# Optimization experiments

Measured on AMD Instinct MI355X. Metric: run time of the kernel, lower is better.

The kernel has to match this reference:

```python
import jax, jax.numpy as jnp
import numpy as np

B, A, T, D = 4, 64, 128, 512
H = 8
DH = D // H
DFF = 4 * D

def layer_norm(x, g, b, eps=1e-5):
    mu = jnp.mean(x, axis=-1, keepdims=True)
    var = jnp.var(x, axis=-1, keepdims=True)
    return (x - mu) * jax.lax.rsqrt(var + eps) * g + b

def setup_inputs() -> dict:
    key = jax.random.key(0)
    ks = jax.random.split(key, 8)
    s = 0.02
    return {
        "x": jax.random.normal(ks[0], (B, A, T, D), dtype=jnp.float32),
        "ln1_g": jnp.ones((D,), jnp.float32),
        "ln1_b": jnp.zeros((D,), jnp.float32),
        "W_qkv": jax.random.normal(ks[1], (D, 3 * D), jnp.float32) * s,
        "b_qkv": jnp.zeros((3 * D,), jnp.float32),
        "W_proj": jax.random.normal(ks[2], (D, D), jnp.float32) * s,
        "b_proj": jnp.zeros((D,), jnp.float32),
        "ln2_g": jnp.ones((D,), jnp.float32),
        "ln2_b": jnp.zeros((D,), jnp.float32),
        "W_fc": jax.random.normal(ks[3], (D, DFF), jnp.float32) * s,
        "b_fc": jnp.zeros((DFF,), jnp.float32),
        "W_out": jax.random.normal(ks[4], (DFF, D), jnp.float32) * s,
        "b_out": jnp.zeros((D,), jnp.float32),
    }

def reference(x, ln1_g, ln1_b, W_qkv, b_qkv, W_proj, b_proj,
              ln2_g, ln2_b, W_fc, b_fc, W_out, b_out):
    # pre-norm (note: original adds residual from the NORMED x)
    xn = layer_norm(x, ln1_g, ln1_b)
    # qkv projection: [B,A,T,3D]
    qkv = xn @ W_qkv + b_qkv
    q, k, v = jnp.split(qkv, 3, axis=-1)
    # [B,A,T,H,DH]
    q = q.reshape(B, A, T, H, DH)
    k = k.reshape(B, A, T, H, DH)
    v = v.reshape(B, A, T, H, DH)
    # attention across time, per (batch, agent, head): scores [B,A,H,T,T]
    att = jnp.einsum('bathd,bashd->bahts', q, k) * (1.0 / np.sqrt(DH))
    causal = jnp.tril(jnp.ones((T, T), dtype=bool))
    att = jnp.where(causal, att, -jnp.inf)
    att = jax.nn.softmax(att, axis=-1)
    y = jnp.einsum('bahts,bashd->bathd', att, v).reshape(B, A, T, D)
    y = y @ W_proj + b_proj
    x = xn + y
    # MLP block
    xn2 = layer_norm(x, ln2_g, ln2_b)
    h = jax.nn.gelu(xn2 @ W_fc + b_fc, approximate=False)
    m = h @ W_out + b_out
    return xn2 + m
```

## Files before the change

kernel.cpp:

```cpp
#include <hip/hip_runtime.h>
#include <math.h>

#define DEV static __device__ __forceinline__

typedef unsigned short u16;
typedef __attribute__((ext_vector_type(8))) short short8;
typedef __attribute__((ext_vector_type(4))) float floatx4;

DEV u16 f2bf(float f) {
  unsigned u = __float_as_uint(f);
  unsigned r = u + 0x7FFFu + ((u >> 16) & 1u);
  return (u16)(r >> 16);
}
DEV float bf2f(u16 v) { return __uint_as_float(((unsigned)v) << 16); }

typedef __attribute__((address_space(1))) void gvoid;
typedef __attribute__((address_space(3))) void lvoid;

DEV void gload16(const u16* g, u16* l) {
  __builtin_amdgcn_global_load_lds((gvoid*)g, (lvoid*)l, 16, 0, 0);
}

__global__ __launch_bounds__(256) void tcast_k(const float* __restrict__ in,
                                               u16* __restrict__ out, int K, int N) {
  __shared__ float t[32][33];
  int nb = blockIdx.x * 32, kb = blockIdx.y * 32;
  int tx = threadIdx.x, ty = threadIdx.y;
#pragma unroll
  for (int r = 0; r < 32; r += 8)
    t[r + ty][tx] = in[(long)(kb + r + ty) * N + nb + tx];
  __syncthreads();
#pragma unroll
  for (int r = 0; r < 32; r += 8)
    out[(long)(nb + r + ty) * K + kb + tx] = f2bf(t[tx][r + ty]);
}

template <typename TI>
__global__ __launch_bounds__(256) void ln_k(const TI* __restrict__ x,
                                            const float* __restrict__ g,
                                            const float* __restrict__ b,
                                            u16* __restrict__ xb) {
  const int lane = threadIdx.x & 63, wid = threadIdx.x >> 6;
  const long row = (long)blockIdx.x * 4 + wid;
  float vv[8];
  if constexpr (sizeof(TI) == 4) {
    const float4* xr = (const float4*)((const float*)x + row * 512);
    float4 v0 = xr[lane * 2], v1 = xr[lane * 2 + 1];
    vv[0] = v0.x; vv[1] = v0.y; vv[2] = v0.z; vv[3] = v0.w;
    vv[4] = v1.x; vv[5] = v1.y; vv[6] = v1.z; vv[7] = v1.w;
  } else {
    short8 v = *(const short8*)((const u16*)x + row * 512 + lane * 8);
#pragma unroll
    for (int i = 0; i < 8; ++i) vv[i] = bf2f((u16)v[i]);
  }
  float s = 0.f, q = 0.f;
#pragma unroll
  for (int i = 0; i < 8; ++i) { s += vv[i]; q += vv[i] * vv[i]; }
#pragma unroll
  for (int off = 1; off < 64; off <<= 1) {
    s += __shfl_xor(s, off, 64);
    q += __shfl_xor(q, off, 64);
  }
  float mean = s * (1.f / 512.f);
  float var = q * (1.f / 512.f) - mean * mean;
  float rs = rsqrtf(var + 1e-5f);
  const float4* gp = (const float4*)g;
  const float4* bp = (const float4*)b;
  float4 g0 = gp[lane * 2], g1 = gp[lane * 2 + 1];
  float4 b0 = bp[lane * 2], b1 = bp[lane * 2 + 1];
  float gg[8] = {g0.x, g0.y, g0.z, g0.w, g1.x, g1.y, g1.z, g1.w};
  float bb[8] = {b0.x, b0.y, b0.z, b0.w, b1.x, b1.y, b1.z, b1.w};
  short8 ov;
#pragma unroll
  for (int i = 0; i < 8; ++i)
    ov[i] = (short)f2bf((vv[i] - mean) * rs * gg[i] + bb[i]);
  *(short8*)&xb[row * 512 + lane * 8] = ov;
}

template <int EPI>
__global__ __launch_bounds__(256) void gemm_k(const u16* __restrict__ A,
                                              const u16* __restrict__ Bt,
                                              const float* __restrict__ bias,
                                              const u16* __restrict__ res,
                                              void* __restrict__ out,
                                              int M, int N, int K) {
  __shared__ __align__(16) u16 lA[128 * 32];
  __shared__ __align__(16) u16 lB[128 * 32];
  const int tid = threadIdx.x;
  const int lane = tid & 63, wid = tid >> 6;
  const int lane15 = lane & 15, khi = lane >> 4;
  const int wr = wid >> 1, wc = wid & 1;
  const long rowB = (long)blockIdx.y * 128;
  const long colB = (long)blockIdx.x * 128;

  floatx4 acc[4][4];
#pragma unroll
  for (int m = 0; m < 4; ++m)
#pragma unroll
    for (int n = 0; n < 4; ++n) acc[m][n] = floatx4{0.f, 0.f, 0.f, 0.f};

  for (int kt = 0; kt < K; kt += 32) {
    __syncthreads();
#pragma unroll
    for (int j = 0; j < 2; ++j) {
      int c = j * 256 + tid;
      int r = c >> 2, cq = c & 3;
      gload16(A + (rowB + r) * K + kt + cq * 8, &lA[(j * 256 + wid * 64) * 8]);
    }
#pragma unroll
    for (int j = 0; j < 2; ++j) {
      int c = j * 256 + tid;
      int r = c >> 2, cq = c & 3;
      gload16(Bt + (colB + r) * K + kt + cq * 8, &lB[(j * 256 + wid * 64) * 8]);
    }
    asm volatile("s_waitcnt vmcnt(0)" ::: "memory");
    __syncthreads();

    short8 af[4];
#pragma unroll
    for (int m = 0; m < 4; ++m)
      af[m] = *(const short8*)&lA[(wr * 64 + m * 16 + lane15) * 32 + khi * 8];
#pragma unroll
    for (int n = 0; n < 4; ++n) {
      short8 bfg = *(const short8*)&lB[(wc * 64 + n * 16 + lane15) * 32 + khi * 8];
#pragma unroll
      for (int m = 0; m < 4; ++m)
        acc[m][n] = __builtin_amdgcn_mfma_f32_16x16x32_bf16(af[m], bfg, acc[m][n], 0, 0, 0);
    }
  }

  const long r0 = rowB + wr * 64;
  const long c0 = colB + wc * 64;
#pragma unroll
  for (int m = 0; m < 4; ++m) {
#pragma unroll
    for (int n = 0; n < 4; ++n) {
      long col = c0 + n * 16 + lane15;
      float bv = bias[col];
#pragma unroll
      for (int jj = 0; jj < 4; ++jj) {
        long row = r0 + m * 16 + khi * 4 + jj;
        float v = acc[m][n][jj] + bv;
        if (EPI == 1) v = 0.5f * v * (1.f + erff(v * 0.70710678118f));
        if (EPI == 2 || EPI == 3) v += bf2f(res[row * N + col]);
        if (EPI == 3) {
          ((float*)out)[row * N + col] = v;
        } else {
          ((u16*)out)[row * N + col] = f2bf(v);
        }
      }
    }
  }
}

__global__ __launch_bounds__(256) void attn_k(const u16* __restrict__ qkv,
                                              u16* __restrict__ y) {
  union U {
    struct { u16 q[128 * 64]; u16 k[128 * 64]; } qk;
    u16 p[128 * 128];
  };
  __shared__ __align__(16) U u;
  __shared__ __align__(16) u16 vt[64 * 128];

  const int tid = threadIdx.x;
  const int lane = tid & 63, wid = tid >> 6;
  const int lane15 = lane & 15, khi = lane >> 4;
  const int h = blockIdx.x & 7;
  const long R0 = (long)(blockIdx.x >> 3) * 128;
  const u16* base = qkv + R0 * 1536 + h * 64;

#pragma unroll
  for (int it = 0; it < 4; ++it) {
    int c = it * 256 + tid;
    int r = c >> 3, ch = c & 7;
    const u16* gq = base + (long)r * 1536 + ch * 8;
    uint4 dq = *(const uint4*)gq;
    uint4 dk = *(const uint4*)(gq + 512);
    uint4 dv = *(const uint4*)(gq + 1024);
    int qi = (r * 64 + ch * 8) ^ ((r & 7) << 3);
    *(uint4*)&u.qk.q[qi] = dq;
    *(uint4*)&u.qk.k[qi] = dk;
    u16 tmp[8];
    *(uint4*)tmp = dv;
#pragma unroll
    for (int i = 0; i < 8; ++i) {
      int d = ch * 8 + i;
      vt[(d * 128 + r) ^ ((d & 7) << 3)] = tmp[i];
    }
  }
  __syncthreads();

  const int r0 = wid * 32;
  floatx4 sc[2][8];
#pragma unroll
  for (int mt = 0; mt < 2; ++mt)
#pragma unroll
    for (int c = 0; c < 8; ++c) sc[mt][c] = floatx4{0.f, 0.f, 0.f, 0.f};

#pragma unroll
  for (int kk = 0; kk < 2; ++kk) {
    short8 aq[2];
#pragma unroll
    for (int mt = 0; mt < 2; ++mt) {
      int rr = r0 + mt * 16 + lane15;
      aq[mt] = *(const short8*)&u.qk.q[(rr * 64 + kk * 32 + khi * 8) ^ ((rr & 7) << 3)];
    }
#pragma unroll
    for (int c = 0; c < 8; ++c) {
      int rk = c * 16 + lane15;
      short8 bk = *(const short8*)&u.qk.k[(rk * 64 + kk * 32 + khi * 8) ^ ((rk & 7) << 3)];
#pragma unroll
      for (int mt = 0; mt < 2; ++mt)
        sc[mt][c] = __builtin_amdgcn_mfma_f32_16x16x32_bf16(aq[mt], bk, sc[mt][c], 0, 0, 0);
    }
  }
  __syncthreads();

#pragma unroll
  for (int mt = 0; mt < 2; ++mt) {
#pragma unroll
    for (int jj = 0; jj < 4; ++jj) {
      int t = r0 + mt * 16 + khi * 4 + jj;
      float vals[8];
      float mx = -1e30f;
#pragma unroll
      for (int c = 0; c < 8; ++c) {
        int s = c * 16 + lane15;
        float v = sc[mt][c][jj] * 0.125f;
        vals[c] = (s <= t) ? v : -1e30f;
        mx = fmaxf(mx, vals[c]);
      }
#pragma unroll
      for (int off = 1; off < 16; off <<= 1) mx = fmaxf(mx, __shfl_xor(mx, off, 64));
      float sum = 0.f;
#pragma unroll
      for (int c = 0; c < 8; ++c) {
        float p = __expf(vals[c] - mx);
        vals[c] = p;
        sum += p;
      }
#pragma unroll
      for (int off = 1; off < 16; off <<= 1) sum += __shfl_xor(sum, off, 64);
      float inv = 1.f / sum;
#pragma unroll
      for (int c = 0; c < 8; ++c) {
        int s = c * 16 + lane15;
        u.p[(t * 128 + s) ^ ((t & 7) << 3)] = f2bf(vals[c] * inv);
      }
    }
  }
  __syncthreads();

  floatx4 ya[2][4];
#pragma unroll
  for (int mt = 0; mt < 2; ++mt)
#pragma unroll
    for (int n = 0; n < 4; ++n) ya[mt][n] = floatx4{0.f, 0.f, 0.f, 0.f};

#pragma unroll
  for (int kk = 0; kk < 4; ++kk) {
    short8 ap[2];
#pragma unroll
    for (int mt = 0; mt < 2; ++mt) {
      int rr = r0 + mt * 16 + lane15;
      ap[mt] = *(const short8*)&u.p[(rr * 128 + kk * 32 + khi * 8) ^ ((rr & 7) << 3)];
    }
#pragma unroll
    for (int n = 0; n < 4; ++n) {
      int d = n * 16 + lane15;
      short8 bv = *(const short8*)&vt[(d * 128 + kk * 32 + khi * 8) ^ ((d & 7) << 3)];
#pragma unroll
      for (int mt = 0; mt < 2; ++mt)
        ya[mt][n] = __builtin_amdgcn_mfma_f32_16x16x32_bf16(ap[mt], bv, ya[mt][n], 0, 0, 0);
    }
  }

  u16* yb = y + R0 * 512 + h * 64;
#pragma unroll
  for (int mt = 0; mt < 2; ++mt)
#pragma unroll
    for (int n = 0; n < 4; ++n)
#pragma unroll
      for (int jj = 0; jj < 4; ++jj) {
        int t = r0 + mt * 16 + khi * 4 + jj;
        int d = n * 16 + lane15;
        yb[(long)t * 512 + d] = f2bf(ya[mt][n][jj]);
      }
}

extern "C" void kernel_launch(void* const* d_in, const int* in_sizes, int n_in,
                              void* d_out, int out_size, void* d_ws, size_t ws_size,
                              hipStream_t stream) {
  const float* x      = (const float*)d_in[0];
  const float* ln1_g  = (const float*)d_in[1];
  const float* ln1_b  = (const float*)d_in[2];
  const float* W_qkv  = (const float*)d_in[3];
  const float* b_qkv  = (const float*)d_in[4];
  const float* W_proj = (const float*)d_in[5];
  const float* b_proj = (const float*)d_in[6];
  const float* ln2_g  = (const float*)d_in[7];
  const float* ln2_b  = (const float*)d_in[8];
  const float* W_fc   = (const float*)d_in[9];
  const float* b_fc   = (const float*)d_in[10];
  const float* W_out  = (const float*)d_in[11];
  const float* b_out  = (const float*)d_in[12];

  const size_t MiB = 1024 * 1024;
  char* ws = (char*)d_ws;
  u16* wq   = (u16*)(ws + 0);
  u16* wp   = (u16*)(ws + 1536 * 512 * 2);
  u16* wf   = (u16*)(ws + 2 * MiB);
  u16* wo   = (u16*)(ws + 4 * MiB);
  u16* xnB  = (u16*)(ws + 8 * MiB);
  u16* qkvB = (u16*)(ws + 40 * MiB);
  u16* yB   = (u16*)(ws + 136 * MiB);
  u16* x2B  = (u16*)(ws + 40 * MiB);
  u16* xn2B = (u16*)(ws + 8 * MiB);
  u16* hB   = (u16*)(ws + 40 * MiB);

  const int M = 32768;

  tcast_k<<<dim3(1536 / 32, 512 / 32), dim3(32, 8), 0, stream>>>(W_qkv, wq, 512, 1536);
  tcast_k<<<dim3(512 / 32, 512 / 32), dim3(32, 8), 0, stream>>>(W_proj, wp, 512, 512);
  tcast_k<<<dim3(2048 / 32, 512 / 32), dim3(32, 8), 0, stream>>>(W_fc, wf, 512, 2048);
  tcast_k<<<dim3(512 / 32, 2048 / 32), dim3(32, 8), 0, stream>>>(W_out, wo, 2048, 512);

  ln_k<float><<<M / 4, 256, 0, stream>>>(x, ln1_g, ln1_b, xnB);
  gemm_k<0><<<dim3(1536 / 128, M / 128), 256, 0, stream>>>(xnB, wq, b_qkv, nullptr,
                                                           qkvB, M, 1536, 512);
  attn_k<<<2048, 256, 0, stream>>>(qkvB, yB);
  gemm_k<2><<<dim3(512 / 128, M / 128), 256, 0, stream>>>(yB, wp, b_proj, xnB,
                                                          x2B, M, 512, 512);
  ln_k<u16><<<M / 4, 256, 0, stream>>>(x2B, ln2_g, ln2_b, xn2B);
  gemm_k<1><<<dim3(2048 / 128, M / 128), 256, 0, stream>>>(xn2B, wf, b_fc, nullptr,
                                                           hB, M, 2048, 512);
  gemm_k<3><<<dim3(512 / 128, M / 128), 256, 0, stream>>>(hB, wo, b_out, xn2B,
                                                          (float*)d_out, M, 512, 2048);
}
```

Baseline: 532.5 us.

## Double-buffer GEMM LDS tiles and remap workgroups for XCD locality

Measured after the change: 507.7 us. -4.7%, faster.

```diff
diff --git a/kernel.cpp b/kernel.cpp
--- a/kernel.cpp
+++ b/kernel.cpp
@@ -84,14 +84,27 @@
                                               const u16* __restrict__ res,
                                               void* __restrict__ out,
                                               int M, int N, int K) {
-  __shared__ __align__(16) u16 lA[128 * 32];
-  __shared__ __align__(16) u16 lB[128 * 32];
+  __shared__ __align__(16) u16 lA[2][128 * 32];
+  __shared__ __align__(16) u16 lB[2][128 * 32];
   const int tid = threadIdx.x;
   const int lane = tid & 63, wid = tid >> 6;
   const int lane15 = lane & 15, khi = lane >> 4;
   const int wr = wid >> 1, wc = wid & 1;
-  const long rowB = (long)blockIdx.y * 128;
-  const long colB = (long)blockIdx.x * 128;
+
+  const int gx = gridDim.x;
+  const int nwg = gx * gridDim.y;
+  const int orig = blockIdx.y * gx + blockIdx.x;
+  const int wgid = (orig & 7) * (nwg >> 3) + (orig >> 3);
+  const int bx = wgid % gx;
+  const int by = wgid / gx;
+
+  const long rowB = (long)by * 128;
+  const long colB = (long)bx * 128;
+
+  const int rr = tid >> 2, cq = tid & 3;
+  const u16* gA0 = A + (rowB + rr) * (long)K + cq * 8;
+  const u16* gB0 = Bt + (colB + rr) * (long)K + cq * 8;
+  const long skip = 64 * (long)K;
 
   floatx4 acc[4][4];
 #pragma unroll
@@ -99,34 +112,35 @@
 #pragma unroll
     for (int n = 0; n < 4; ++n) acc[m][n] = floatx4{0.f, 0.f, 0.f, 0.f};
 
-  for (int kt = 0; kt < K; kt += 32) {
-    __syncthreads();
-#pragma unroll
-    for (int j = 0; j < 2; ++j) {
-      int c = j * 256 + tid;
-      int r = c >> 2, cq = c & 3;
-      gload16(A + (rowB + r) * K + kt + cq * 8, &lA[(j * 256 + wid * 64) * 8]);
-    }
-#pragma unroll
-    for (int j = 0; j < 2; ++j) {
-      int c = j * 256 + tid;
-      int r = c >> 2, cq = c & 3;
-      gload16(Bt + (colB + r) * K + kt + cq * 8, &lB[(j * 256 + wid * 64) * 8]);
+  auto stage = [&](int buf, int kt) {
+    gload16(gA0 + kt, &lA[buf][(wid * 64) * 8]);
+    gload16(gA0 + skip + kt, &lA[buf][(256 + wid * 64) * 8]);
+    gload16(gB0 + kt, &lB[buf][(wid * 64) * 8]);
+    gload16(gB0 + skip + kt, &lB[buf][(256 + wid * 64) * 8]);
+  };
+
+  stage(0, 0);
+  asm volatile("s_waitcnt vmcnt(0)" ::: "memory");
+  __syncthreads();
+
+  const int nt = K >> 5;
+  for (int t = 0; t < nt; ++t) {
+    const int cur = t & 1;
+    if (t + 1 < nt) stage(cur ^ 1, (t + 1) << 5);
+    __builtin_amdgcn_sched_barrier(0);
+    short8 af[4];
+#pragma unroll
+    for (int m = 0; m < 4; ++m)
+      af[m] = *(const short8*)&lA[cur][(wr * 64 + m * 16 + lane15) * 32 + khi * 8];
+#pragma unroll
+    for (int n = 0; n < 4; ++n) {
+      short8 bfg = *(const short8*)&lB[cur][(wc * 64 + n * 16 + lane15) * 32 + khi * 8];
+#pragma unroll
+      for (int m = 0; m < 4; ++m)
+        acc[m][n] = __builtin_amdgcn_mfma_f32_16x16x32_bf16(af[m], bfg, acc[m][n], 0, 0, 0);
     }
     asm volatile("s_waitcnt vmcnt(0)" ::: "memory");
     __syncthreads();
-
-    short8 af[4];
-#pragma unroll
-    for (int m = 0; m < 4; ++m)
-      af[m] = *(const short8*)&lA[(wr * 64 + m * 16 + lane15) * 32 + khi * 8];
-#pragma unroll
-    for (int n = 0; n < 4; ++n) {
-      short8 bfg = *(const short8*)&lB[(wc * 64 + n * 16 + lane15) * 32 + khi * 8];
-#pragma unroll
-      for (int m = 0; m < 4; ++m)
-        acc[m][n] = __builtin_amdgcn_mfma_f32_16x16x32_bf16(af[m], bfg, acc[m][n], 0, 0, 0);
-    }
   }
 
   const long r0 = rowB + wr * 64;
```

## Rewrite GEMM as 256x256 tile with 4-stage LDS pipeline and swizzle

Applied to the files above, without the earlier changes.

Measured after the change: 475.7 us. 1.12x faster.

```diff
diff --git a/kernel.cpp b/kernel.cpp
--- a/kernel.cpp
+++ b/kernel.cpp
@@ -78,61 +78,111 @@
 }
 
 template <int EPI>
-__global__ __launch_bounds__(256) void gemm_k(const u16* __restrict__ A,
+__global__ __launch_bounds__(512) void gemm_k(const u16* __restrict__ A,
                                               const u16* __restrict__ Bt,
                                               const float* __restrict__ bias,
                                               const u16* __restrict__ res,
                                               void* __restrict__ out,
                                               int M, int N, int K) {
-  __shared__ __align__(16) u16 lA[128 * 32];
-  __shared__ __align__(16) u16 lB[128 * 32];
+  __shared__ __align__(16) u16 ls[4][2][256 * 32];
   const int tid = threadIdx.x;
-  const int lane = tid & 63, wid = tid >> 6;
+  const int lane = tid & 63, w = tid >> 6;
   const int lane15 = lane & 15, khi = lane >> 4;
-  const int wr = wid >> 1, wc = wid & 1;
-  const long rowB = (long)blockIdx.y * 128;
-  const long colB = (long)blockIdx.x * 128;
-
-  floatx4 acc[4][4];
-#pragma unroll
-  for (int m = 0; m < 4; ++m)
+  const int wr = w >> 2, wcn = w & 3;
+
+  const int gx = gridDim.x;
+  const int nwg = gx * gridDim.y;
+  const int orig = blockIdx.y * gx + blockIdx.x;
+  const int wgid = (orig & 7) * (nwg >> 3) + (orig >> 3);
+  const int bx = wgid % gx, by = wgid / gx;
+  const long rowB = (long)by * 256, colB = (long)bx * 256;
+
+  const int sr = w * 16 + (lane >> 2);
+  const int scb = (lane & 3) * 16;
+
+  auto stageA = [&](int b, int kt) {
+#pragma unroll
+    for (int j = 0; j < 2; ++j) {
+      int r = j * 128 + sr;
+      int sw = ((r >> 1) & 3) << 4;
+      gload16(A + (rowB + r) * (long)K + kt * 32 + ((scb ^ sw) >> 1),
+              &ls[b][0][j * 4096 + w * 512]);
+    }
+  };
+  auto stageB = [&](int b, int kt) {
+#pragma unroll
+    for (int j = 0; j < 2; ++j) {
+      int r = j * 128 + sr;
+      int sw = ((r >> 1) & 3) << 4;
+      gload16(Bt + (colB + r) * (long)K + kt * 32 + ((scb ^ sw) >> 1),
+              &ls[b][1][j * 4096 + w * 512]);
+    }
+  };
+  auto rdA = [&](int b, int m) -> short8 {
+    int r = wr * 128 + m * 16 + lane15;
+    int c8 = (khi ^ ((r >> 1) & 3)) * 8;
+    return *(const short8*)&ls[b][0][r * 32 + c8];
+  };
+  auto rdB = [&](int b, int n) -> short8 {
+    int r = wcn * 64 + n * 16 + lane15;
+    int c8 = (khi ^ ((r >> 1) & 3)) * 8;
+    return *(const short8*)&ls[b][1][r * 32 + c8];
+  };
+
+  floatx4 acc[8][4];
+#pragma unroll
+  for (int m = 0; m < 8; ++m)
 #pragma unroll
     for (int n = 0; n < 4; ++n) acc[m][n] = floatx4{0.f, 0.f, 0.f, 0.f};
 
-  for (int kt = 0; kt < K; kt += 32) {
-    __syncthreads();
-#pragma unroll
-    for (int j = 0; j < 2; ++j) {
-      int c = j * 256 + tid;
-      int r = c >> 2, cq = c & 3;
-      gload16(A + (rowB + r) * K + kt + cq * 8, &lA[(j * 256 + wid * 64) * 8]);
-    }
-#pragma unroll
-    for (int j = 0; j < 2; ++j) {
-      int c = j * 256 + tid;
-      int r = c >> 2, cq = c & 3;
-      gload16(Bt + (colB + r) * K + kt + cq * 8, &lB[(j * 256 + wid * 64) * 8]);
-    }
-    asm volatile("s_waitcnt vmcnt(0)" ::: "memory");
-    __syncthreads();
-
-    short8 af[4];
-#pragma unroll
-    for (int m = 0; m < 4; ++m)
-      af[m] = *(const short8*)&lA[(wr * 64 + m * 16 + lane15) * 32 + khi * 8];
-#pragma unroll
-    for (int n = 0; n < 4; ++n) {
-      short8 bfg = *(const short8*)&lB[(wc * 64 + n * 16 + lane15) * 32 + khi * 8];
+  stageA(0, 0); stageB(0, 0);
+  stageA(1, 1); stageB(1, 1);
+  asm volatile("s_waitcnt vmcnt(4)" ::: "memory");
+  __builtin_amdgcn_s_barrier();
+
+  const int NT = K >> 5;
+  for (int t = 0; t < NT; ++t) {
+    const int b = t & 3;
+    short8 bfr[4], afr[4];
+#pragma unroll
+    for (int n = 0; n < 4; ++n) bfr[n] = rdB(b, n);
+#pragma unroll
+    for (int m = 0; m < 4; ++m) afr[m] = rdA(b, m);
+    if (t + 2 < NT) stageA((t + 2) & 3, t + 2);
+    __builtin_amdgcn_sched_barrier(0);
+    __builtin_amdgcn_s_barrier();
+    __builtin_amdgcn_s_setprio(1);
+#pragma unroll
+    for (int n = 0; n < 4; ++n)
 #pragma unroll
       for (int m = 0; m < 4; ++m)
-        acc[m][n] = __builtin_amdgcn_mfma_f32_16x16x32_bf16(af[m], bfg, acc[m][n], 0, 0, 0);
-    }
-  }
-
-  const long r0 = rowB + wr * 64;
-  const long c0 = colB + wc * 64;
-#pragma unroll
-  for (int m = 0; m < 4; ++m) {
+        acc[m][n] = __builtin_amdgcn_mfma_f32_16x16x32_bf16(afr[m], bfr[n], acc[m][n], 0, 0, 0);
+    __builtin_amdgcn_s_setprio(0);
+    __builtin_amdgcn_s_barrier();
+#pragma unroll
+    for (int m = 0; m < 4; ++m) afr[m] = rdA(b, m + 4);
+    if (t + 2 < NT) stageB((t + 2) & 3, t + 2);
+    __builtin_amdgcn_sched_barrier(0);
+    __builtin_amdgcn_s_barrier();
+    __builtin_amdgcn_s_setprio(1);
+#pragma unroll
+    for (int n = 0; n < 4; ++n)
+#pragma unroll
+      for (int m = 0; m < 4; ++m)
+        acc[m + 4][n] = __builtin_amdgcn_mfma_f32_16x16x32_bf16(afr[m], bfr[n], acc[m + 4][n], 0, 0, 0);
+    __builtin_amdgcn_s_setprio(0);
+    if (t + 2 < NT) {
+      asm volatile("s_waitcnt vmcnt(4)" ::: "memory");
+    } else if (t + 1 < NT) {
+      asm volatile("s_waitcnt vmcnt(0)" ::: "memory");
+    }
+    __builtin_amdgcn_s_barrier();
+  }
+
+  const long r0 = rowB + wr * 128;
+  const long c0 = colB + wcn * 64;
+#pragma unroll
+  for (int m = 0; m < 8; ++m) {
 #pragma unroll
     for (int n = 0; n < 4; ++n) {
       long col = c0 + n * 16 + lane15;
@@ -326,14 +376,14 @@
   tcast_k<<<dim3(512 / 32, 2048 / 32), dim3(32, 8), 0, stream>>>(W_out, wo, 2048, 512);
 
   ln_k<float><<<M / 4, 256, 0, stream>>>(x, ln1_g, ln1_b, xnB);
-  gemm_k<0><<<dim3(1536 / 128, M / 128), 256, 0, stream>>>(xnB, wq, b_qkv, nullptr,
+  gemm_k<0><<<dim3(1536 / 256, M / 256), 512, 0, stream>>>(xnB, wq, b_qkv, nullptr,
                                                            qkvB, M, 1536, 512);
   attn_k<<<2048, 256, 0, stream>>>(qkvB, yB);
-  gemm_k<2><<<dim3(512 / 128, M / 128), 256, 0, stream>>>(yB, wp, b_proj, xnB,
+  gemm_k<2><<<dim3(512 / 256, M / 256), 512, 0, stream>>>(yB, wp, b_proj, xnB,
                                                           x2B, M, 512, 512);
   ln_k<u16><<<M / 4, 256, 0, stream>>>(x2B, ln2_g, ln2_b, xn2B);
-  gemm_k<1><<<dim3(2048 / 128, M / 128), 256, 0, stream>>>(xn2B, wf, b_fc, nullptr,
+  gemm_k<1><<<dim3(2048 / 256, M / 256), 512, 0, stream>>>(xn2B, wf, b_fc, nullptr,
                                                            hB, M, 2048, 512);
-  gemm_k<3><<<dim3(512 / 128, M / 128), 256, 0, stream>>>(hB, wo, b_out, xn2B,
+  gemm_k<3><<<dim3(512 / 256, M / 256), 512, 0, stream>>>(hB, wo, b_out, xn2B,
                                                           (float*)d_out, M, 512, 2048);
 }
```

## Deepen GEMM K-tile to 64 with XOR-swizzled LDS and grouped block remap

Applied to the files above, without the earlier changes.

Result: faster. 446.6 us (-16.1%).

```diff
diff --git a/kernel.cpp b/kernel.cpp
--- a/kernel.cpp
+++ b/kernel.cpp
@@ -78,20 +78,35 @@
 }
 
 template <int EPI>
-__global__ __launch_bounds__(256) void gemm_k(const u16* __restrict__ A,
-                                              const u16* __restrict__ Bt,
-                                              const float* __restrict__ bias,
-                                              const u16* __restrict__ res,
-                                              void* __restrict__ out,
-                                              int M, int N, int K) {
-  __shared__ __align__(16) u16 lA[128 * 32];
-  __shared__ __align__(16) u16 lB[128 * 32];
+__global__ __launch_bounds__(256, 4) void gemm_k(const u16* __restrict__ A,
+                                                 const u16* __restrict__ Bt,
+                                                 const float* __restrict__ bias,
+                                                 const u16* __restrict__ res,
+                                                 void* __restrict__ out,
+                                                 int M, int N, int K) {
+  __shared__ __align__(16) u16 lA[128 * 64];
+  __shared__ __align__(16) u16 lB[128 * 64];
   const int tid = threadIdx.x;
-  const int lane = tid & 63, wid = tid >> 6;
+  const int lane = tid & 63, w = tid >> 6;
   const int lane15 = lane & 15, khi = lane >> 4;
-  const int wr = wid >> 1, wc = wid & 1;
-  const long rowB = (long)blockIdx.y * 128;
-  const long colB = (long)blockIdx.x * 128;
+  const int wr = w >> 1, wc = w & 1;
+
+  const int gx = gridDim.x;
+  const int nwg = gx * gridDim.y;
+  const int orig = blockIdx.y * gx + blockIdx.x;
+  const int wgid = (orig & 7) * (nwg >> 3) + (orig >> 3);
+  const int bx = wgid % gx, by = wgid / gx;
+  const long rowB = (long)by * 128, colB = (long)bx * 128;
+
+  const int srow = w * 32 + (lane >> 3);
+  const int sswz = ((lane & 7) ^ (lane >> 3)) * 8;
+  const u16* gA0 = A + (rowB + srow) * (long)K + sswz;
+  const u16* gB0 = Bt + (colB + srow) * (long)K + sswz;
+  const long j8K = 8 * (long)K;
+
+  const int rx = lane15 & 7;
+  const int s0 = (khi ^ rx) * 8;
+  const int s1 = ((4 + khi) ^ rx) * 8;
 
   floatx4 acc[4][4];
 #pragma unroll
@@ -99,33 +114,32 @@
 #pragma unroll
     for (int n = 0; n < 4; ++n) acc[m][n] = floatx4{0.f, 0.f, 0.f, 0.f};
 
-  for (int kt = 0; kt < K; kt += 32) {
+  const int NT = K >> 6;
+  for (int t = 0; t < NT; ++t) {
+    const long kt = (long)t << 6;
     __syncthreads();
 #pragma unroll
-    for (int j = 0; j < 2; ++j) {
-      int c = j * 256 + tid;
-      int r = c >> 2, cq = c & 3;
-      gload16(A + (rowB + r) * K + kt + cq * 8, &lA[(j * 256 + wid * 64) * 8]);
-    }
-#pragma unroll
-    for (int j = 0; j < 2; ++j) {
-      int c = j * 256 + tid;
-      int r = c >> 2, cq = c & 3;
-      gload16(Bt + (colB + r) * K + kt + cq * 8, &lB[(j * 256 + wid * 64) * 8]);
+    for (int j = 0; j < 4; ++j) {
+      gload16(gA0 + j * j8K + kt, &lA[(w * 4 + j) * 512]);
+      gload16(gB0 + j * j8K + kt, &lB[(w * 4 + j) * 512]);
     }
     asm volatile("s_waitcnt vmcnt(0)" ::: "memory");
     __syncthreads();
 
-    short8 af[4];
-#pragma unroll
-    for (int m = 0; m < 4; ++m)
-      af[m] = *(const short8*)&lA[(wr * 64 + m * 16 + lane15) * 32 + khi * 8];
-#pragma unroll
-    for (int n = 0; n < 4; ++n) {
-      short8 bfg = *(const short8*)&lB[(wc * 64 + n * 16 + lane15) * 32 + khi * 8];
+#pragma unroll
+    for (int kk = 0; kk < 2; ++kk) {
+      const int sk = kk ? s1 : s0;
+      short8 af[4];
 #pragma unroll
       for (int m = 0; m < 4; ++m)
-        acc[m][n] = __builtin_amdgcn_mfma_f32_16x16x32_bf16(af[m], bfg, acc[m][n], 0, 0, 0);
+        af[m] = *(const short8*)&lA[(wr * 64 + m * 16 + lane15) * 64 + sk];
+#pragma unroll
+      for (int n = 0; n < 4; ++n) {
+        short8 bfg = *(const short8*)&lB[(wc * 64 + n * 16 + lane15) * 64 + sk];
+#pragma unroll
+        for (int m = 0; m < 4; ++m)
+          acc[m][n] = __builtin_amdgcn_mfma_f32_16x16x32_bf16(af[m], bfg, acc[m][n], 0, 0, 0);
+      }
     }
   }
 
```
